# Kernel tuning notes

Measured on AMD Instinct MI355X. Metric: run time of the kernel, lower is better.

The kernel has to match this reference:

```python
import jax, jax.numpy as jnp
import numpy as np

B, NIN, NOUT, CIN, COUT = 32, 512, 128, 128, 32
NUM_ITERS = 10


def setup_inputs() -> dict:
    key = jax.random.key(0)
    k1, k2, k3 = jax.random.split(key, 3)
    x = jax.random.normal(k1, (B, NIN, CIN), dtype=jnp.float32)
    y = jax.random.randint(k2, (B,), 0, NOUT)  # unused by forward, kept for signature fidelity
    # xavier_uniform over W1 [1,Nin,Nout,Cout,Cin] (torch fan_in=Nin*Nout*Cout... use gain-1 approx on last two dims)
    limit = float(np.sqrt(6.0 / (CIN + COUT)))
    W1 = jax.random.uniform(k3, (NIN, NOUT, COUT, CIN), dtype=jnp.float32, minval=-limit, maxval=limit)
    return {"x": x, "W1": W1, "y": y}


def _forward(x, W1):
    # u_hat[b,n,m,o] = sum_c W1[n,m,o,c] * x[b,n,c]   -- per-(in,out) capsule linear transform
    u_hat = jnp.einsum('nmoc,bnc->bnmo', W1, x)  # [B, Nin, Nout, Cout]
    b0 = jnp.zeros(u_hat.shape[:3], dtype=u_hat.dtype)  # [B, Nin, Nout]

    def step(b, _):
        c = jax.nn.softmax(b, axis=2)                        # route weights over output capsules
        s = jnp.einsum('bnm,bnmo->bmo', c, u_hat)            # weighted sum over input capsules
        # squash_v1 with axis=1 on a singleton dim in the original -> elementwise degenerate form
        s2 = s * s
        v = (jnp.sqrt(s2) / (0.5 + s2)) * s                  # [B, Nout, Cout]
        agree = jnp.einsum('bmo,bnmo->bnm', v, u_hat)        # agreement update
        return b + agree, v

    _, vs = jax.lax.scan(step, b0, None, length=NUM_ITERS)
    poses = vs[-1]                                            # [B, Nout, Cout]
    activations = jnp.sqrt(jnp.sum(poses * poses, axis=2))    # [B, Nout]
    return poses, activations


def reference(x, W1, y):
    return _forward(x, W1)
```

## Files before the change

kernel.cpp:

```cpp
#include <hip/hip_runtime.h>
#include <hip/hip_bf16.h>
#include <stdint.h>
#include <math.h>

#define NIN_  512
#define NOUT_ 128
#define CIN_  128
#define COUT_ 32
#define MO_   4096
#define NBT_  32
#define RB_   16
#define NQ2_  32

typedef __attribute__((ext_vector_type(4))) float f32x4;

__global__ __launch_bounds__(256) void k_build(const float* __restrict__ x,
                                               const float* __restrict__ W1,
                                               float* __restrict__ u) {
    const int n   = blockIdx.x >> 4;
    const int mt  = blockIdx.x & 15;
    const int mo0 = mt * 256;
    const int t   = threadIdx.x;
    const int l   = t & 63;
    const int bg  = t >> 6;

    __shared__ f32x4 xs4[32 * 32];
    __shared__ f32x4 ws4[256 * 8];

    for (int k = t; k < NBT_ * 32; k += 256) {
        const int bl = k >> 5;
        const int cu = k & 31;
        xs4[k] = *(const f32x4*)(x + (((size_t)bl * NIN_ + n) * CIN_ + cu * 4));
    }

    const int cu8 = t & 7;
    const int row = t >> 3;

    float acc[4][8];
#pragma unroll
    for (int i = 0; i < 4; ++i)
#pragma unroll
        for (int j = 0; j < 8; ++j) acc[i][j] = 0.f;

    f32x4 wr[8];
#pragma unroll
    for (int p = 0; p < 8; ++p) {
        const int ml = row + p * 32;
        wr[p] = *(const f32x4*)(W1 + ((size_t)(n * MO_ + mo0 + ml) * CIN_ + 0 * 32 + cu8 * 4));
    }

    for (int ch = 0; ch < 4; ++ch) {
        __syncthreads();
#pragma unroll
        for (int p = 0; p < 8; ++p) {
            const int ml = row + p * 32;
            ws4[ml * 8 + (cu8 ^ (ml & 7))] = wr[p];
        }
        __syncthreads();
        if (ch < 3) {
#pragma unroll
            for (int p = 0; p < 8; ++p) {
                const int ml = row + p * 32;
                wr[p] = *(const f32x4*)(W1 + ((size_t)(n * MO_ + mo0 + ml) * CIN_ + (ch + 1) * 32 + cu8 * 4));
            }
        }
#pragma unroll
        for (int c4 = 0; c4 < 8; ++c4) {
            f32x4 wv[4];
#pragma unroll
            for (int i = 0; i < 4; ++i)
                wv[i] = ws4[(l + i * 64) * 8 + (c4 ^ (l & 7))];
            f32x4 xq[8];
#pragma unroll
            for (int j = 0; j < 8; ++j)
                xq[j] = xs4[(bg * 8 + j) * 32 + ch * 8 + c4];
#pragma unroll
            for (int i = 0; i < 4; ++i)
#pragma unroll
                for (int j = 0; j < 8; ++j) {
                    acc[i][j] += wv[i][0] * xq[j][0];
                    acc[i][j] += wv[i][1] * xq[j][1];
                    acc[i][j] += wv[i][2] * xq[j][2];
                    acc[i][j] += wv[i][3] * xq[j][3];
                }
        }
    }

#pragma unroll
    for (int i = 0; i < 4; ++i)
#pragma unroll
        for (int j = 0; j < 8; ++j)
            u[((size_t)n * NBT_ + bg * 8 + j) * MO_ + mo0 + i * 64 + l] = acc[i][j];
}

__global__ __launch_bounds__(256) void k_mean(const float* __restrict__ u,
                                              float* __restrict__ vws, int bofs) {
    const int j  = blockIdx.x * 256 + threadIdx.x;
    const int bl = j >> 12;
    const int mo = j & (MO_ - 1);
    const float* up = u + (size_t)(bofs + bl) * MO_ + mo;
    float s = 0.f;
#pragma unroll 8
    for (int n = 0; n < NIN_; ++n) s += up[(size_t)n * NBT_ * MO_];
    s *= (1.0f / 128.0f);
    const float s2 = s * s;
    vws[j] = (sqrtf(s2) / (0.5f + s2)) * s;
}

template<int MODE>
__global__ __launch_bounds__(256) void k_route(const float* __restrict__ u,
                                               const float* __restrict__ vws,
                                               float* __restrict__ blog,
                                               float* __restrict__ spart,
                                               int bofs) {
    const int bl  = blockIdx.x & 15;
    const int qq  = blockIdx.x >> 4;
    const int w   = threadIdx.x >> 6;
    const int l   = threadIdx.x & 63;
    const int sub = l >> 3;

    __shared__ f32x4 lred[4][16][64];

    f32x4 vr[16];
#pragma unroll
    for (int j = 0; j < 16; ++j)
        vr[j] = *(const f32x4*)(vws + (size_t)bl * MO_ + (j * 64 + l) * 4);

    f32x4 sacc[16];
#pragma unroll
    for (int j = 0; j < 16; ++j) sacc[j] = (f32x4){0.f, 0.f, 0.f, 0.f};

    for (int nn = 0; nn < 4; ++nn) {
        const int n = qq * 16 + w * 4 + nn;
        const f32x4* up = (const f32x4*)(u + ((size_t)n * NBT_ + bofs + bl) * MO_);
        f32x4 ur[16];
#pragma unroll
        for (int j = 0; j < 16; ++j) ur[j] = up[j * 64 + l];

        float* bp = blog + ((size_t)bl * NIN_ + n) * NOUT_;
        float bn[16];
        float mx = -1e30f;
#pragma unroll
        for (int j = 0; j < 16; ++j) {
            float p = vr[j][0] * ur[j][0] + vr[j][1] * ur[j][1]
                    + vr[j][2] * ur[j][2] + vr[j][3] * ur[j][3];
            p += __shfl_xor(p, 1, 64);
            p += __shfl_xor(p, 2, 64);
            p += __shfl_xor(p, 4, 64);
            const float old = (MODE == 1) ? 0.f : bp[j * 8 + sub];
            bn[j] = old + p;
            mx = fmaxf(mx, bn[j]);
        }
        if ((l & 7) == 0) {
#pragma unroll
            for (int j = 0; j < 16; ++j) bp[j * 8 + sub] = bn[j];
        }
        mx = fmaxf(mx, __shfl_xor(mx, 8, 64));
        mx = fmaxf(mx, __shfl_xor(mx, 16, 64));
        mx = fmaxf(mx, __shfl_xor(mx, 32, 64));
        float se = 0.f;
#pragma unroll
        for (int j = 0; j < 16; ++j) {
            bn[j] = expf(bn[j] - mx);
            se += bn[j];
        }
        se += __shfl_xor(se, 8, 64);
        se += __shfl_xor(se, 16, 64);
        se += __shfl_xor(se, 32, 64);
        const float inv = 1.0f / se;
#pragma unroll
        for (int j = 0; j < 16; ++j) {
            const float c = bn[j] * inv;
            sacc[j][0] += c * ur[j][0]; sacc[j][1] += c * ur[j][1];
            sacc[j][2] += c * ur[j][2]; sacc[j][3] += c * ur[j][3];
        }
    }

#pragma unroll
    for (int j = 0; j < 16; ++j) lred[w][j][l] = sacc[j];
    __syncthreads();

    f32x4* sp = (f32x4*)(spart + ((size_t)qq * RB_ + bl) * MO_);
#pragma unroll
    for (int jj = 0; jj < 4; ++jj) {
        const int j = w * 4 + jj;
        const f32x4 a0 = lred[0][j][l];
        const f32x4 a1 = lred[1][j][l];
        const f32x4 a2 = lred[2][j][l];
        const f32x4 a3 = lred[3][j][l];
        f32x4 r;
#pragma unroll
        for (int c = 0; c < 4; ++c) r[c] = ((a0[c] + a1[c]) + a2[c]) + a3[c];
        sp[j * 64 + l] = r;
    }
}

__global__ __launch_bounds__(256) void k_squash_mid(const float* __restrict__ spart,
                                                    float* __restrict__ vws) {
    const int j = blockIdx.x * 256 + threadIdx.x;
    const size_t stride = (size_t)RB_ * MO_;
    float s = 0.f;
#pragma unroll 8
    for (int q = 0; q < NQ2_; ++q) s += spart[q * stride + j];
    const float s2 = s * s;
    vws[j] = (sqrtf(s2) / (0.5f + s2)) * s;
}

__global__ __launch_bounds__(256) void k_squash_fin(const float* __restrict__ spart,
                                                    float* __restrict__ out,
                                                    int b0) {
    const int j = blockIdx.x * 256 + threadIdx.x;
    const size_t stride = (size_t)RB_ * MO_;
    float s = 0.f;
#pragma unroll 8
    for (int q = 0; q < NQ2_; ++q) s += spart[q * stride + j];
    const float s2 = s * s;
    const float v = (sqrtf(s2) / (0.5f + s2)) * s;
    out[(size_t)b0 * MO_ + j] = v;

    float v2 = v * v;
#pragma unroll
    for (int d = 16; d >= 1; d >>= 1) v2 += __shfl_xor(v2, d, 64);
    if ((j & 31) == 0) {
        const int bl = j >> 12;
        const int m  = (j >> 5) & 127;
        out[131072 + (size_t)(b0 + bl) * NOUT_ + m] = sqrtf(v2);
    }
}

extern "C" void kernel_launch(void* const* d_in, const int* in_sizes, int n_in,
                              void* d_out, int out_size, void* d_ws, size_t ws_size,
                              hipStream_t stream) {
    const float* x  = (const float*)d_in[0];
    const float* W1 = (const float*)d_in[1];
    float* out = (float*)d_out;

    char* ws = (char*)d_ws;
    const size_t bytes_u  = (size_t)NBT_ * NIN_ * MO_ * 4;
    const size_t bytes_bl = (size_t)RB_ * NIN_ * NOUT_ * 4;
    const size_t bytes_v  = (size_t)RB_ * MO_ * 4;
    const size_t bytes_sp = (size_t)NQ2_ * RB_ * MO_ * 4;
    const size_t need = bytes_u + bytes_bl + bytes_v + bytes_sp;
    if (ws_size < need) return;

    float* u     = (float*)(ws);
    float* blog  = (float*)(ws + bytes_u);
    float* vws   = (float*)(ws + bytes_u + bytes_bl);
    float* spart = (float*)(ws + bytes_u + bytes_bl + bytes_v);

    k_build<<<8192, 256, 0, stream>>>(x, W1, u);

    const int rgrid = RB_ * NQ2_;
    const int sgrid = (RB_ * MO_) / 256;

    for (int h = 0; h < 2; ++h) {
        const int bofs = h * RB_;

        k_mean<<<sgrid, 256, 0, stream>>>(u, vws, bofs);

        for (int it = 1; it <= 9; ++it) {
            if (it == 1) k_route<1><<<rgrid, 256, 0, stream>>>(u, vws, blog, spart, bofs);
            else         k_route<2><<<rgrid, 256, 0, stream>>>(u, vws, blog, spart, bofs);
            if (it < 9) k_squash_mid<<<sgrid, 256, 0, stream>>>(spart, vws);
            else        k_squash_fin<<<sgrid, 256, 0, stream>>>(spart, out, bofs);
        }
    }
}
```

Measured before the change: 927.4 us.

## Fuse routing iterations into persistent kernel with per-batch grid barriers

Replaces the per-iteration launches of mean, route and squash kernels with one persistent kernel per batch half. Each batch's 32 blocks synchronize through a software barrier built on global atomic counters, and the squash reduction is done by a few threads of each block between barriers. This removes about 40 kernel launches and their inter-kernel gaps. In exchange it relies on all 512 blocks being co-resident to avoid deadlock, and it adds atomic spin-wait latency at each barrier.

```diff
diff --git a/kernel.cpp b/kernel.cpp
--- a/kernel.cpp
+++ b/kernel.cpp
@@ -93,138 +93,168 @@
             u[((size_t)n * NBT_ + bg * 8 + j) * MO_ + mo0 + i * 64 + l] = acc[i][j];
 }
 
-__global__ __launch_bounds__(256) void k_mean(const float* __restrict__ u,
-                                              float* __restrict__ vws, int bofs) {
-    const int j  = blockIdx.x * 256 + threadIdx.x;
-    const int bl = j >> 12;
-    const int mo = j & (MO_ - 1);
-    const float* up = u + (size_t)(bofs + bl) * MO_ + mo;
-    float s = 0.f;
+static __device__ __forceinline__ void gbar(unsigned* cnt, unsigned* gen) {
+    __syncthreads();
+    if (threadIdx.x == 0) {
+        __threadfence();
+        const unsigned g = atomicAdd(gen, 0u);
+        const unsigned a = atomicAdd(cnt, 1u);
+        if (a == 31u) {
+            atomicExch(cnt, 0u);
+            __threadfence();
+            atomicAdd(gen, 1u);
+        } else {
+            while (atomicAdd(gen, 0u) == g) { __builtin_amdgcn_s_sleep(2); }
+        }
+        __threadfence();
+    }
+    __syncthreads();
+}
+
+__global__ __launch_bounds__(256, 2) void k_routeloop(const float* __restrict__ u,
+                                                      float* __restrict__ vws,
+                                                      float* __restrict__ blog,
+                                                      float* __restrict__ spart,
+                                                      float* __restrict__ out,
+                                                      unsigned* __restrict__ ctrl,
+                                                      int bofs) {
+    const int bid = blockIdx.x;
+    const int bl  = bid >> 5;
+    const int qq  = bid & 31;
+    const int t   = threadIdx.x;
+    const int w   = t >> 6;
+    const int l   = t & 63;
+    const int sub = l >> 3;
+
+    unsigned* cnt = ctrl + bl * 64;
+    unsigned* gen = cnt + 1;
+
+    __shared__ f32x4 lred[4][16][64];
+
+    {
+        const int mo   = qq * 128 + (t >> 1);
+        const int half = t & 1;
+        const float* up = u + (size_t)(bofs + bl) * MO_ + mo;
+        float p = 0.f;
 #pragma unroll 8
-    for (int n = 0; n < NIN_; ++n) s += up[(size_t)n * NBT_ * MO_];
-    s *= (1.0f / 128.0f);
-    const float s2 = s * s;
-    vws[j] = (sqrtf(s2) / (0.5f + s2)) * s;
-}
-
-template<int MODE>
-__global__ __launch_bounds__(256) void k_route(const float* __restrict__ u,
-                                               const float* __restrict__ vws,
-                                               float* __restrict__ blog,
-                                               float* __restrict__ spart,
-                                               int bofs) {
-    const int bl  = blockIdx.x & 15;
-    const int qq  = blockIdx.x >> 4;
-    const int w   = threadIdx.x >> 6;
-    const int l   = threadIdx.x & 63;
-    const int sub = l >> 3;
-
-    __shared__ f32x4 lred[4][16][64];
-
-    f32x4 vr[16];
-#pragma unroll
-    for (int j = 0; j < 16; ++j)
-        vr[j] = *(const f32x4*)(vws + (size_t)bl * MO_ + (j * 64 + l) * 4);
-
-    f32x4 sacc[16];
-#pragma unroll
-    for (int j = 0; j < 16; ++j) sacc[j] = (f32x4){0.f, 0.f, 0.f, 0.f};
-
-    for (int nn = 0; nn < 4; ++nn) {
-        const int n = qq * 16 + w * 4 + nn;
-        const f32x4* up = (const f32x4*)(u + ((size_t)n * NBT_ + bofs + bl) * MO_);
-        f32x4 ur[16];
-#pragma unroll
-        for (int j = 0; j < 16; ++j) ur[j] = up[j * 64 + l];
-
-        float* bp = blog + ((size_t)bl * NIN_ + n) * NOUT_;
-        float bn[16];
-        float mx = -1e30f;
-#pragma unroll
-        for (int j = 0; j < 16; ++j) {
-            float p = vr[j][0] * ur[j][0] + vr[j][1] * ur[j][1]
-                    + vr[j][2] * ur[j][2] + vr[j][3] * ur[j][3];
-            p += __shfl_xor(p, 1, 64);
-            p += __shfl_xor(p, 2, 64);
-            p += __shfl_xor(p, 4, 64);
-            const float old = (MODE == 1) ? 0.f : bp[j * 8 + sub];
-            bn[j] = old + p;
-            mx = fmaxf(mx, bn[j]);
-        }
-        if ((l & 7) == 0) {
-#pragma unroll
-            for (int j = 0; j < 16; ++j) bp[j * 8 + sub] = bn[j];
-        }
-        mx = fmaxf(mx, __shfl_xor(mx, 8, 64));
-        mx = fmaxf(mx, __shfl_xor(mx, 16, 64));
-        mx = fmaxf(mx, __shfl_xor(mx, 32, 64));
-        float se = 0.f;
-#pragma unroll
-        for (int j = 0; j < 16; ++j) {
-            bn[j] = expf(bn[j] - mx);
-            se += bn[j];
-        }
-        se += __shfl_xor(se, 8, 64);
-        se += __shfl_xor(se, 16, 64);
-        se += __shfl_xor(se, 32, 64);
-        const float inv = 1.0f / se;
-#pragma unroll
-        for (int j = 0; j < 16; ++j) {
-            const float c = bn[j] * inv;
-            sacc[j][0] += c * ur[j][0]; sacc[j][1] += c * ur[j][1];
-            sacc[j][2] += c * ur[j][2]; sacc[j][3] += c * ur[j][3];
-        }
-    }
-
-#pragma unroll
-    for (int j = 0; j < 16; ++j) lred[w][j][l] = sacc[j];
-    __syncthreads();
-
-    f32x4* sp = (f32x4*)(spart + ((size_t)qq * RB_ + bl) * MO_);
-#pragma unroll
-    for (int jj = 0; jj < 4; ++jj) {
-        const int j = w * 4 + jj;
-        const f32x4 a0 = lred[0][j][l];
-        const f32x4 a1 = lred[1][j][l];
-        const f32x4 a2 = lred[2][j][l];
-        const f32x4 a3 = lred[3][j][l];
-        f32x4 r;
-#pragma unroll
-        for (int c = 0; c < 4; ++c) r[c] = ((a0[c] + a1[c]) + a2[c]) + a3[c];
-        sp[j * 64 + l] = r;
-    }
-}
-
-__global__ __launch_bounds__(256) void k_squash_mid(const float* __restrict__ spart,
-                                                    float* __restrict__ vws) {
-    const int j = blockIdx.x * 256 + threadIdx.x;
-    const size_t stride = (size_t)RB_ * MO_;
-    float s = 0.f;
+        for (int n = half * 256; n < half * 256 + 256; ++n)
+            p += up[(size_t)n * NBT_ * MO_];
+        const float pp = p + __shfl_xor(p, 1, 64);
+        if (half == 0) {
+            const float s = pp * (1.0f / 128.0f);
+            const float s2 = s * s;
+            vws[bl * MO_ + mo] = (sqrtf(s2) / (0.5f + s2)) * s;
+        }
+    }
+    gbar(cnt, gen);
+
+    for (int it = 1; it <= 9; ++it) {
+        f32x4 vr[16];
+#pragma unroll
+        for (int j = 0; j < 16; ++j)
+            vr[j] = *(const f32x4*)(vws + (size_t)bl * MO_ + (j * 64 + l) * 4);
+
+        f32x4 sacc[16];
+#pragma unroll
+        for (int j = 0; j < 16; ++j) sacc[j] = (f32x4){0.f, 0.f, 0.f, 0.f};
+
+        for (int nn = 0; nn < 4; ++nn) {
+            const int n = qq * 16 + w * 4 + nn;
+            const f32x4* up = (const f32x4*)(u + ((size_t)n * NBT_ + bofs + bl) * MO_);
+            f32x4 ur[16];
+#pragma unroll
+            for (int j = 0; j < 16; ++j) ur[j] = up[j * 64 + l];
+
+            float* bp = blog + ((size_t)bl * NIN_ + n) * NOUT_;
+            float bn[16];
+            float mx = -1e30f;
+#pragma unroll
+            for (int j = 0; j < 16; ++j) {
+                float p = vr[j][0] * ur[j][0] + vr[j][1] * ur[j][1]
+                        + vr[j][2] * ur[j][2] + vr[j][3] * ur[j][3];
+                p += __shfl_xor(p, 1, 64);
+                p += __shfl_xor(p, 2, 64);
+                p += __shfl_xor(p, 4, 64);
+                const float old = (it == 1) ? 0.f : bp[j * 8 + sub];
+                bn[j] = old + p;
+                mx = fmaxf(mx, bn[j]);
+            }
+            if ((l & 7) == 0) {
+#pragma unroll
+                for (int j = 0; j < 16; ++j) bp[j * 8 + sub] = bn[j];
+            }
+            mx = fmaxf(mx, __shfl_xor(mx, 8, 64));
+            mx = fmaxf(mx, __shfl_xor(mx, 16, 64));
+            mx = fmaxf(mx, __shfl_xor(mx, 32, 64));
+            float se = 0.f;
+#pragma unroll
+            for (int j = 0; j < 16; ++j) {
+                bn[j] = expf(bn[j] - mx);
+                se += bn[j];
+            }
+            se += __shfl_xor(se, 8, 64);
+            se += __shfl_xor(se, 16, 64);
+            se += __shfl_xor(se, 32, 64);
+            const float inv = 1.0f / se;
+#pragma unroll
+            for (int j = 0; j < 16; ++j) {
+                const float c = bn[j] * inv;
+                sacc[j][0] += c * ur[j][0]; sacc[j][1] += c * ur[j][1];
+                sacc[j][2] += c * ur[j][2]; sacc[j][3] += c * ur[j][3];
+            }
+        }
+
+#pragma unroll
+        for (int j = 0; j < 16; ++j) lred[w][j][l] = sacc[j];
+        __syncthreads();
+
+        f32x4* sp = (f32x4*)(spart + ((size_t)qq * RB_ + bl) * MO_);
+#pragma unroll
+        for (int jj = 0; jj < 4; ++jj) {
+            const int j = w * 4 + jj;
+            const f32x4 a0 = lred[0][j][l];
+            const f32x4 a1 = lred[1][j][l];
+            const f32x4 a2 = lred[2][j][l];
+            const f32x4 a3 = lred[3][j][l];
+            f32x4 r;
+#pragma unroll
+            for (int c = 0; c < 4; ++c) r[c] = ((a0[c] + a1[c]) + a2[c]) + a3[c];
+            sp[j * 64 + l] = r;
+        }
+        gbar(cnt, gen);
+
+        if (t < 32) {
+            const int uidx = qq * 32 + t;
+            const f32x4* sp4 = (const f32x4*)spart;
+            const size_t stride4 = (size_t)RB_ * MO_ / 4;
+            const size_t base4   = ((size_t)bl * MO_) / 4 + uidx;
+            f32x4 s = {0.f, 0.f, 0.f, 0.f};
 #pragma unroll 8
-    for (int q = 0; q < NQ2_; ++q) s += spart[q * stride + j];
-    const float s2 = s * s;
-    vws[j] = (sqrtf(s2) / (0.5f + s2)) * s;
-}
-
-__global__ __launch_bounds__(256) void k_squash_fin(const float* __restrict__ spart,
-                                                    float* __restrict__ out,
-                                                    int b0) {
-    const int j = blockIdx.x * 256 + threadIdx.x;
-    const size_t stride = (size_t)RB_ * MO_;
-    float s = 0.f;
-#pragma unroll 8
-    for (int q = 0; q < NQ2_; ++q) s += spart[q * stride + j];
-    const float s2 = s * s;
-    const float v = (sqrtf(s2) / (0.5f + s2)) * s;
-    out[(size_t)b0 * MO_ + j] = v;
-
-    float v2 = v * v;
-#pragma unroll
-    for (int d = 16; d >= 1; d >>= 1) v2 += __shfl_xor(v2, d, 64);
-    if ((j & 31) == 0) {
-        const int bl = j >> 12;
-        const int m  = (j >> 5) & 127;
-        out[131072 + (size_t)(b0 + bl) * NOUT_ + m] = sqrtf(v2);
+            for (int q = 0; q < NQ2_; ++q) {
+                const f32x4 vq = sp4[q * stride4 + base4];
+                s[0] += vq[0]; s[1] += vq[1]; s[2] += vq[2]; s[3] += vq[3];
+            }
+            f32x4 v;
+#pragma unroll
+            for (int c = 0; c < 4; ++c) {
+                const float s2 = s[c] * s[c];
+                v[c] = (sqrtf(s2) / (0.5f + s2)) * s[c];
+            }
+            if (it < 9) {
+                ((f32x4*)vws)[((size_t)bl * MO_) / 4 + uidx] = v;
+            } else {
+                ((f32x4*)out)[((size_t)(bofs + bl) * MO_) / 4 + uidx] = v;
+                float v2 = v[0] * v[0] + v[1] * v[1] + v[2] * v[2] + v[3] * v[3];
+                v2 += __shfl_xor(v2, 1, 64);
+                v2 += __shfl_xor(v2, 2, 64);
+                v2 += __shfl_xor(v2, 4, 64);
+                if ((t & 7) == 0) {
+                    const int m = uidx >> 3;
+                    out[131072 + (size_t)(bofs + bl) * NOUT_ + m] = sqrtf(v2);
+                }
+            }
+        }
+        if (it < 9) gbar(cnt, gen);
     }
 }
 
@@ -240,29 +270,20 @@
     const size_t bytes_bl = (size_t)RB_ * NIN_ * NOUT_ * 4;
     const size_t bytes_v  = (size_t)RB_ * MO_ * 4;
     const size_t bytes_sp = (size_t)NQ2_ * RB_ * MO_ * 4;
-    const size_t need = bytes_u + bytes_bl + bytes_v + bytes_sp;
+    const size_t bytes_ct = 16 * 64 * sizeof(unsigned);
+    const size_t need = bytes_u + bytes_bl + bytes_v + bytes_sp + bytes_ct;
     if (ws_size < need) return;
 
-    float* u     = (float*)(ws);
-    float* blog  = (float*)(ws + bytes_u);
-    float* vws   = (float*)(ws + bytes_u + bytes_bl);
-    float* spart = (float*)(ws + bytes_u + bytes_bl + bytes_v);
+    float*    u     = (float*)(ws);
+    float*    blog  = (float*)(ws + bytes_u);
+    float*    vws   = (float*)(ws + bytes_u + bytes_bl);
+    float*    spart = (float*)(ws + bytes_u + bytes_bl + bytes_v);
+    unsigned* ctrl  = (unsigned*)(ws + bytes_u + bytes_bl + bytes_v + bytes_sp);
+
+    hipMemsetAsync(ctrl, 0, bytes_ct, stream);
 
     k_build<<<8192, 256, 0, stream>>>(x, W1, u);
 
-    const int rgrid = RB_ * NQ2_;
-    const int sgrid = (RB_ * MO_) / 256;
-
-    for (int h = 0; h < 2; ++h) {
-        const int bofs = h * RB_;
-
-        k_mean<<<sgrid, 256, 0, stream>>>(u, vws, bofs);
-
-        for (int it = 1; it <= 9; ++it) {
-            if (it == 1) k_route<1><<<rgrid, 256, 0, stream>>>(u, vws, blog, spart, bofs);
-            else         k_route<2><<<rgrid, 256, 0, stream>>>(u, vws, blog, spart, bofs);
-            if (it < 9) k_squash_mid<<<sgrid, 256, 0, stream>>>(spart, vws);
-            else        k_squash_fin<<<sgrid, 256, 0, stream>>>(spart, out, bofs);
-        }
-    }
-}
+    k_routeloop<<<RB_ * NQ2_, 256, 0, stream>>>(u, vws, blog, spart, out, ctrl, 0);
+    k_routeloop<<<RB_ * NQ2_, 256, 0, stream>>>(u, vws, blog, spart, out, ctrl, RB_);
+}
```

After: 2.047 ms. +120.7%, slower.
